# Performance work log

Hardware: AMD Instinct MI355X
Metric: run time of the kernel (lower is better)

The kernel has to match this reference:

```python
import jax, jax.numpy as jnp
import numpy as np

B = 64      # batch
T = 32      # frames per clip
H = 256     # hidden_dim
NMAX = 64   # max boxes per batch element


def _n_per_frame():
    rng = np.random.default_rng(0)
    return rng.integers(32, NMAX + 1, size=B)  # each n <= NMAX


def setup_inputs() -> dict:
    n = _n_per_frame()
    N = int(n.sum())  # total boxes across batch (~3072)
    key = jax.random.key(0)
    k1, k2, k3 = jax.random.split(key, 3)
    bbox = jax.random.uniform(k1, (N * T, 4), dtype=jnp.float32)
    W1 = jax.random.normal(k2, (4, 128), dtype=jnp.float32) * 0.5
    b1 = jnp.zeros((128,), jnp.float32)
    W2 = jax.random.normal(k3, (128, H), dtype=jnp.float32) * 0.0884  # ~1/sqrt(128)
    b2 = jnp.zeros((H,), jnp.float32)
    return {
        "bbox": bbox,
        "W1": W1, "b1": b1, "W2": W2, "b2": b2,
        "n_per_frame": jnp.asarray(n, jnp.int32),
        "n_max": NMAX,
    }


def reference(bbox, W1, b1, W2, b2, n_per_frame, n_max):
    N = bbox.shape[0] // T  # static total box count
    # tiny MLP: 4 -> 128 -> H
    pos = (jax.nn.relu(bbox @ W1 + b1) @ W2 + b2).reshape(N, T, H)
    # ragged scatter into padded (B*n_max, T, H) tensor
    frame_id = jnp.repeat(jnp.arange(B), n_per_frame, total_repeat_length=N)  # [N]
    starts = jnp.cumsum(n_per_frame) - n_per_frame                            # exclusive cumsum [B]
    local = jnp.arange(N) - starts[frame_id]                                  # slot within frame
    tgt = frame_id * n_max + local                                            # [N] unique targets
    pos_pad = jnp.zeros((B * n_max, T, H), pos.dtype).at[tgt].set(pos)
    # (B, n_max, T, H) -> (B, T, n_max, H) -> (B*T, n_max, H) -> (n_max, B*T, H)
    out = (pos_pad.reshape(B, n_max, T, H)
           .transpose(0, 2, 1, 3)
           .reshape(B * T, n_max, H)
           .transpose(1, 0, 2))
    return out
```

## Files before the change

kernel.cpp:

```cpp
#include <hip/hip_runtime.h>

#define B_ 64
#define T_ 32
#define H_ 256
#define NMAX_ 64
#define TILES 2048
#define GRID 512
#define BLOCK 256
#define SROW 260

typedef __attribute__((ext_vector_type(8))) short short8;
typedef __attribute__((ext_vector_type(4))) float f32x4;

__device__ __forceinline__ short f2bf(float f) {
    unsigned u = __builtin_bit_cast(unsigned, f);
    u = (u + 0x7fffu + ((u >> 16) & 1u)) >> 16;
    return (short)u;
}

__device__ __forceinline__ void barrier_nodrain() {
    asm volatile("s_waitcnt lgkmcnt(0)\n\ts_barrier" ::: "memory");
}

__global__ __launch_bounds__(BLOCK, 2)
void pe_fused(const float* __restrict__ bbox,
              const float* __restrict__ W1,
              const float* __restrict__ b1,
              const float* __restrict__ W2,
              const float* __restrict__ b2,
              const int*   __restrict__ npf,
              float* __restrict__ out,
              int NT)
{
    __shared__ float W1s[512];
    __shared__ float b1s[128];
    __shared__ int   s_n[64];
    __shared__ int   s_start[64];
    __shared__ short Hs[64 * 136];
    __shared__ float stage[32 * SROW];

    const int tid  = threadIdx.x;
    const int wave = tid >> 6;
    const int lane = tid & 63;
    const int q    = lane >> 4;
    const int m16  = lane & 15;

    if (tid < 256) { W1s[tid] = W1[tid]; W1s[tid + 256] = W1[tid + 256]; }
    if (tid < 128) b1s[tid] = b1[tid];

    if (wave == 0) {
        int v = npf[lane];
        s_n[lane] = v;
        int s = v;
#pragma unroll
        for (int d = 1; d < 64; d <<= 1) {
            int u = __shfl_up(s, d, 64);
            if (lane >= d) s += u;
        }
        s_start[lane] = s - v;
    }

    short8 Wf[4][4];
    float4 b2q[4];
#pragma unroll
    for (int ct = 0; ct < 4; ++ct) {
        b2q[ct] = *(const float4*)(b2 + wave * 64 + ct * 16 + q * 4);
#pragma unroll
        for (int kc = 0; kc < 4; ++kc) {
            const int k0 = kc * 32 + q * 8;
            short8 f;
#pragma unroll
            for (int jj = 0; jj < 8; ++jj)
                f[jj] = f2bf(W2[(k0 + jj) * H_ + wave * 64 + ct * 16 + m16]);
            Wf[ct][kc] = f;
        }
    }
    __syncthreads();

    const int r4 = tid >> 2;
    const int c4 = tid & 3;

    float4 bb[4];
#pragma unroll
    for (int i = 0; i < 4; ++i) {
        const int tt = blockIdx.x + i * GRID;
        const int b  = tt >> 5;
        const int l0 = (tt & 31) * 2;
        const int g  = (s_start[b] + l0) * T_ + r4;
        bb[i] = make_float4(0.f, 0.f, 0.f, 0.f);
        if (g < NT) bb[i] = *(const float4*)(bbox + g * 4);
    }

#pragma unroll
    for (int i = 0; i < 4; ++i) {
        const int tt = blockIdx.x + i * GRID;
        const int b  = tt >> 5;
        const int l0 = (tt & 31) * 2;
        const int nb = s_n[b];

        const int ob0 = (l0 * (B_ * T_) + b * T_) * H_;
        const int ob1 = ob0 + (B_ * T_) * H_;

        if (l0 >= nb) {
            const float4 z = make_float4(0.f, 0.f, 0.f, 0.f);
#pragma unroll
            for (int rr = 0; rr < 16; ++rr) {
                const int r = rr * 4 + wave;
                float* dst = out + (r < 32 ? ob0 + r * H_ : ob1 + (r - 32) * H_);
                *(float4*)(dst + lane * 4) = z;
            }
            continue;
        }

        {
            const float4 bv = bb[i];
            short* hrow = &Hs[r4 * 136 + c4 * 32];
#pragma unroll
            for (int w = 0; w < 4; ++w) {
                short8 hv;
#pragma unroll
                for (int jj = 0; jj < 8; ++jj) {
                    const int h = c4 * 32 + w * 8 + jj;
                    float v = b1s[h];
                    v = fmaf(bv.x, W1s[h],       v);
                    v = fmaf(bv.y, W1s[128 + h], v);
                    v = fmaf(bv.z, W1s[256 + h], v);
                    v = fmaf(bv.w, W1s[384 + h], v);
                    v = fmaxf(v, 0.f);
                    hv[jj] = f2bf(v);
                }
                *(short8*)(hrow + w * 8) = hv;
            }
        }
        barrier_nodrain();

        f32x4 acc[4][4];
#pragma unroll
        for (int ct = 0; ct < 4; ++ct)
#pragma unroll
            for (int rt = 0; rt < 4; ++rt)
                acc[ct][rt] = (f32x4){0.f, 0.f, 0.f, 0.f};

#pragma unroll
        for (int kc = 0; kc < 4; ++kc) {
            short8 hf[4];
#pragma unroll
            for (int rt = 0; rt < 4; ++rt)
                hf[rt] = *(const short8*)&Hs[(rt * 16 + m16) * 136 + kc * 32 + q * 8];
#pragma unroll
            for (int ct = 0; ct < 4; ++ct)
#pragma unroll
                for (int rt = 0; rt < 4; ++rt)
                    acc[ct][rt] = __builtin_amdgcn_mfma_f32_16x16x32_bf16(
                        Wf[ct][kc], hf[rt], acc[ct][rt], 0, 0, 0);
        }

        const bool v1 = (l0 + 1) < nb;
#pragma unroll
        for (int half = 0; half < 2; ++half) {
            const int obh = half ? ob1 : ob0;
            if (half == 1 && !v1) {
                const float4 z = make_float4(0.f, 0.f, 0.f, 0.f);
#pragma unroll
                for (int j = 0; j < 8; ++j)
                    *(float4*)(out + obh + (wave * 8 + j) * H_ + lane * 4) = z;
                continue;
            }
#pragma unroll
            for (int rt2 = 0; rt2 < 2; ++rt2) {
                const int rt = 2 * half + rt2;
                const int u  = rt2 * 16 + m16;
#pragma unroll
                for (int ct = 0; ct < 4; ++ct) {
                    const f32x4 d = acc[ct][rt];
                    float4 v = make_float4(d[0] + b2q[ct].x, d[1] + b2q[ct].y,
                                           d[2] + b2q[ct].z, d[3] + b2q[ct].w);
                    *(float4*)&stage[u * SROW + wave * 64 + ct * 16 + q * 4] = v;
                }
            }
            barrier_nodrain();
#pragma unroll
            for (int j = 0; j < 8; ++j) {
                const int u = wave * 8 + j;
                const float4 v = *(const float4*)&stage[u * SROW + lane * 4];
                *(float4*)(out + obh + u * H_ + lane * 4) = v;
            }
            barrier_nodrain();
        }
    }
}

extern "C" void kernel_launch(void* const* d_in, const int* in_sizes, int n_in,
                              void* d_out, int out_size, void* d_ws, size_t ws_size,
                              hipStream_t stream)
{
    const float* bbox = (const float*)d_in[0];
    const float* W1   = (const float*)d_in[1];
    const float* b1   = (const float*)d_in[2];
    const float* W2   = (const float*)d_in[3];
    const float* b2   = (const float*)d_in[4];
    const int*   npf  = (const int*)d_in[5];
    const int NT = in_sizes[0] / 4;

    pe_fused<<<GRID, BLOCK, 0, stream>>>(bbox, W1, b1, W2, b2, npf,
                                         (float*)d_out, NT);
}
```

Before: 152.6 us.

## Split output columns across block pairs and store MFMA results directly

Raises the grid from 512 to 2048 blocks. Each pair of blocks now splits the 256 output columns into two halves, so each block runs two tile iterations instead of four, with half as many W2 fragments and accumulators held in registers. The LDS staging buffer and its barriers before the global stores are removed, and accumulators are written straight to global memory as 16-byte stores. Accumulators start from b2, and W1 is packed as float4 in LDS. The trade-offs are less coalesced stores (16 rows of 64-byte segments per wave instruction), the layer-1 MLP computed twice per tile (once per column half), and no bbox prefetch across iterations.

```diff
diff --git a/kernel.cpp b/kernel.cpp
--- a/kernel.cpp
+++ b/kernel.cpp
@@ -4,10 +4,9 @@
 #define T_ 32
 #define H_ 256
 #define NMAX_ 64
-#define TILES 2048
-#define GRID 512
+#define GRID 2048
 #define BLOCK 256
-#define SROW 260
+#define HSROW 136
 
 typedef __attribute__((ext_vector_type(8))) short short8;
 typedef __attribute__((ext_vector_type(4))) float f32x4;
@@ -22,7 +21,7 @@
     asm volatile("s_waitcnt lgkmcnt(0)\n\ts_barrier" ::: "memory");
 }
 
-__global__ __launch_bounds__(BLOCK, 2)
+__global__ __launch_bounds__(BLOCK, 4)
 void pe_fused(const float* __restrict__ bbox,
               const float* __restrict__ W1,
               const float* __restrict__ b1,
@@ -32,12 +31,11 @@
               float* __restrict__ out,
               int NT)
 {
-    __shared__ float W1s[512];
-    __shared__ float b1s[128];
-    __shared__ int   s_n[64];
-    __shared__ int   s_start[64];
-    __shared__ short Hs[64 * 136];
-    __shared__ float stage[32 * SROW];
+    __shared__ float4 W1t[128];
+    __shared__ float  b1s[128];
+    __shared__ int    s_n[64];
+    __shared__ int    s_start[64];
+    __shared__ short  Hs[64 * HSROW];
 
     const int tid  = threadIdx.x;
     const int wave = tid >> 6;
@@ -45,9 +43,13 @@
     const int q    = lane >> 4;
     const int m16  = lane & 15;
 
-    if (tid < 256) { W1s[tid] = W1[tid]; W1s[tid + 256] = W1[tid + 256]; }
-    if (tid < 128) b1s[tid] = b1[tid];
+    const int ch = blockIdx.x & 1;
+    const int p0 = blockIdx.x >> 1;
 
+    if (tid < 128) {
+        W1t[tid] = make_float4(W1[tid], W1[128 + tid], W1[256 + tid], W1[384 + tid]);
+        b1s[tid] = b1[tid];
+    }
     if (wave == 0) {
         int v = npf[lane];
         s_n[lane] = v;
@@ -60,72 +62,68 @@
         s_start[lane] = s - v;
     }
 
-    short8 Wf[4][4];
-    float4 b2q[4];
+    const int colw = ch * 128 + wave * 32;
+    short8 Wf[2][4];
 #pragma unroll
-    for (int ct = 0; ct < 4; ++ct) {
-        b2q[ct] = *(const float4*)(b2 + wave * 64 + ct * 16 + q * 4);
+    for (int ct = 0; ct < 2; ++ct)
 #pragma unroll
         for (int kc = 0; kc < 4; ++kc) {
-            const int k0 = kc * 32 + q * 8;
             short8 f;
 #pragma unroll
             for (int jj = 0; jj < 8; ++jj)
-                f[jj] = f2bf(W2[(k0 + jj) * H_ + wave * 64 + ct * 16 + m16]);
+                f[jj] = f2bf(W2[(kc * 32 + q * 8 + jj) * H_ + colw + ct * 16 + m16]);
             Wf[ct][kc] = f;
         }
-    }
-    __syncthreads();
+    float4 b2v[2];
+#pragma unroll
+    for (int ct = 0; ct < 2; ++ct)
+        b2v[ct] = *(const float4*)(b2 + colw + ct * 16 + q * 4);
 
-    const int r4 = tid >> 2;
-    const int c4 = tid & 3;
-
-    float4 bb[4];
-#pragma unroll
-    for (int i = 0; i < 4; ++i) {
-        const int tt = blockIdx.x + i * GRID;
-        const int b  = tt >> 5;
-        const int l0 = (tt & 31) * 2;
-        const int g  = (s_start[b] + l0) * T_ + r4;
-        bb[i] = make_float4(0.f, 0.f, 0.f, 0.f);
-        if (g < NT) bb[i] = *(const float4*)(bbox + g * 4);
-    }
+    barrier_nodrain();
 
 #pragma unroll
-    for (int i = 0; i < 4; ++i) {
-        const int tt = blockIdx.x + i * GRID;
-        const int b  = tt >> 5;
-        const int l0 = (tt & 31) * 2;
-        const int nb = s_n[b];
+    for (int it = 0; it < 2; ++it) {
+        const int pair = it ? (p0 + 1024) : p0;
+        const int b    = pair >> 5;
+        const int l0   = (pair & 31) * 2;
+        const int nb   = s_n[b];
 
         const int ob0 = (l0 * (B_ * T_) + b * T_) * H_;
         const int ob1 = ob0 + (B_ * T_) * H_;
 
         if (l0 >= nb) {
             const float4 z = make_float4(0.f, 0.f, 0.f, 0.f);
+            const int col = ch * 128 + (lane & 31) * 4;
 #pragma unroll
-            for (int rr = 0; rr < 16; ++rr) {
-                const int r = rr * 4 + wave;
-                float* dst = out + (r < 32 ? ob0 + r * H_ : ob1 + (r - 32) * H_);
-                *(float4*)(dst + lane * 4) = z;
+            for (int j = 0; j < 8; ++j) {
+                const int r = wave * 16 + j * 2 + (lane >> 5);
+                float* dst = out + (r < 32 ? ob0 + r * H_ : ob1 + (r - 32) * H_) + col;
+                *(float4*)dst = z;
             }
             continue;
         }
 
+        barrier_nodrain();
+
         {
-            const float4 bv = bb[i];
-            short* hrow = &Hs[r4 * 136 + c4 * 32];
+            const int r4 = tid >> 2;
+            const int c4 = tid & 3;
+            const int g  = (s_start[b] + l0) * T_ + r4;
+            float4 bv = make_float4(0.f, 0.f, 0.f, 0.f);
+            if (g < NT) bv = *(const float4*)(bbox + g * 4);
+            short* hrow = &Hs[r4 * HSROW + c4 * 32];
 #pragma unroll
             for (int w = 0; w < 4; ++w) {
                 short8 hv;
 #pragma unroll
                 for (int jj = 0; jj < 8; ++jj) {
                     const int h = c4 * 32 + w * 8 + jj;
+                    const float4 wv = W1t[h];
                     float v = b1s[h];
-                    v = fmaf(bv.x, W1s[h],       v);
-                    v = fmaf(bv.y, W1s[128 + h], v);
-                    v = fmaf(bv.z, W1s[256 + h], v);
-                    v = fmaf(bv.w, W1s[384 + h], v);
+                    v = fmaf(bv.x, wv.x, v);
+                    v = fmaf(bv.y, wv.y, v);
+                    v = fmaf(bv.z, wv.z, v);
+                    v = fmaf(bv.w, wv.w, v);
                     v = fmaxf(v, 0.f);
                     hv[jj] = f2bf(v);
                 }
@@ -134,21 +132,21 @@
         }
         barrier_nodrain();
 
-        f32x4 acc[4][4];
+        f32x4 acc[2][4];
 #pragma unroll
-        for (int ct = 0; ct < 4; ++ct)
+        for (int ct = 0; ct < 2; ++ct)
 #pragma unroll
             for (int rt = 0; rt < 4; ++rt)
-                acc[ct][rt] = (f32x4){0.f, 0.f, 0.f, 0.f};
+                acc[ct][rt] = (f32x4){b2v[ct].x, b2v[ct].y, b2v[ct].z, b2v[ct].w};
 
 #pragma unroll
         for (int kc = 0; kc < 4; ++kc) {
             short8 hf[4];
 #pragma unroll
             for (int rt = 0; rt < 4; ++rt)
-                hf[rt] = *(const short8*)&Hs[(rt * 16 + m16) * 136 + kc * 32 + q * 8];
+                hf[rt] = *(const short8*)&Hs[(rt * 16 + m16) * HSROW + kc * 32 + q * 8];
 #pragma unroll
-            for (int ct = 0; ct < 4; ++ct)
+            for (int ct = 0; ct < 2; ++ct)
 #pragma unroll
                 for (int rt = 0; rt < 4; ++rt)
                     acc[ct][rt] = __builtin_amdgcn_mfma_f32_16x16x32_bf16(
@@ -157,35 +155,21 @@
 
         const bool v1 = (l0 + 1) < nb;
 #pragma unroll
-        for (int half = 0; half < 2; ++half) {
-            const int obh = half ? ob1 : ob0;
-            if (half == 1 && !v1) {
-                const float4 z = make_float4(0.f, 0.f, 0.f, 0.f);
+        for (int ct = 0; ct < 2; ++ct) {
+            const int cb = colw + ct * 16 + q * 4;
 #pragma unroll
-                for (int j = 0; j < 8; ++j)
-                    *(float4*)(out + obh + (wave * 8 + j) * H_ + lane * 4) = z;
-                continue;
+            for (int rt = 0; rt < 4; ++rt) {
+                const int t = (rt & 1) * 16 + m16;
+                float* dst = out + (rt < 2 ? ob0 : ob1) + t * H_ + cb;
+                float4 val;
+                if (rt >= 2 && !v1) {
+                    val = make_float4(0.f, 0.f, 0.f, 0.f);
+                } else {
+                    const f32x4 a = acc[ct][rt];
+                    val = make_float4(a[0], a[1], a[2], a[3]);
+                }
+                *(float4*)dst = val;
             }
-#pragma unroll
-            for (int rt2 = 0; rt2 < 2; ++rt2) {
-                const int rt = 2 * half + rt2;
-                const int u  = rt2 * 16 + m16;
-#pragma unroll
-                for (int ct = 0; ct < 4; ++ct) {
-                    const f32x4 d = acc[ct][rt];
-                    float4 v = make_float4(d[0] + b2q[ct].x, d[1] + b2q[ct].y,
-                                           d[2] + b2q[ct].z, d[3] + b2q[ct].w);
-                    *(float4*)&stage[u * SROW + wave * 64 + ct * 16 + q * 4] = v;
-                }
-            }
-            barrier_nodrain();
-#pragma unroll
-            for (int j = 0; j < 8; ++j) {
-                const int u = wave * 8 + j;
-                const float4 v = *(const float4*)&stage[u * SROW + lane * 4];
-                *(float4*)(out + obh + u * H_ + lane * 4) = v;
-            }
-            barrier_nodrain();
         }
     }
 }
```

New measurement: 165.4 us. 1.08x slower.

## Alias H and staging LDS buffers, raise occupancy, and double grid size

Applied to the files above, without the earlier changes.

Shares one LDS buffer between the bf16 hidden activations and the output staging area, with an extra barrier after the MFMA loop so the buffer can be reused safely. This cuts LDS per block so three blocks per CU fit, and the grid doubles to 1024 blocks with two tiles each. Other changes: the bias b2 moves into LDS and seeds the accumulators, and W1 is stored transposed as float4 so each hidden value needs one LDS load. The trade-off is an extra barrier per tile, the W2 fragment load and bf16 conversion done by twice as many blocks, and register pressure under the tighter launch bound.

```diff
diff --git a/kernel.cpp b/kernel.cpp
--- a/kernel.cpp
+++ b/kernel.cpp
@@ -4,9 +4,9 @@
 #define T_ 32
 #define H_ 256
 #define NMAX_ 64
-#define TILES 2048
-#define GRID 512
+#define GRID 1024
 #define BLOCK 256
+#define HSROW 136
 #define SROW 260
 
 typedef __attribute__((ext_vector_type(8))) short short8;
@@ -22,7 +22,7 @@
     asm volatile("s_waitcnt lgkmcnt(0)\n\ts_barrier" ::: "memory");
 }
 
-__global__ __launch_bounds__(BLOCK, 2)
+__global__ __launch_bounds__(BLOCK, 3)
 void pe_fused(const float* __restrict__ bbox,
               const float* __restrict__ W1,
               const float* __restrict__ b1,
@@ -32,12 +32,15 @@
               float* __restrict__ out,
               int NT)
 {
-    __shared__ float W1s[512];
-    __shared__ float b1s[128];
-    __shared__ int   s_n[64];
-    __shared__ int   s_start[64];
-    __shared__ short Hs[64 * 136];
-    __shared__ float stage[32 * SROW];
+    __shared__ float4 W1t[128];
+    __shared__ float  b1s[128];
+    __shared__ float  b2s[256];
+    __shared__ int    s_n[64];
+    __shared__ int    s_start[64];
+    __shared__ float  smem[32 * SROW];
+
+    short* const Hs    = (short*)smem;
+    float* const stage = smem;
 
     const int tid  = threadIdx.x;
     const int wave = tid >> 6;
@@ -45,9 +48,11 @@
     const int q    = lane >> 4;
     const int m16  = lane & 15;
 
-    if (tid < 256) { W1s[tid] = W1[tid]; W1s[tid + 256] = W1[tid + 256]; }
-    if (tid < 128) b1s[tid] = b1[tid];
-
+    if (tid < 128) {
+        W1t[tid] = make_float4(W1[tid], W1[128 + tid], W1[256 + tid], W1[384 + tid]);
+        b1s[tid] = b1[tid];
+    }
+    b2s[tid] = b2[tid];
     if (wave == 0) {
         int v = npf[lane];
         s_n[lane] = v;
@@ -61,10 +66,8 @@
     }
 
     short8 Wf[4][4];
-    float4 b2q[4];
-#pragma unroll
-    for (int ct = 0; ct < 4; ++ct) {
-        b2q[ct] = *(const float4*)(b2 + wave * 64 + ct * 16 + q * 4);
+#pragma unroll
+    for (int ct = 0; ct < 4; ++ct)
 #pragma unroll
         for (int kc = 0; kc < 4; ++kc) {
             const int k0 = kc * 32 + q * 8;
@@ -74,15 +77,14 @@
                 f[jj] = f2bf(W2[(k0 + jj) * H_ + wave * 64 + ct * 16 + m16]);
             Wf[ct][kc] = f;
         }
-    }
     __syncthreads();
 
     const int r4 = tid >> 2;
     const int c4 = tid & 3;
 
-    float4 bb[4];
-#pragma unroll
-    for (int i = 0; i < 4; ++i) {
+    float4 bb[2];
+#pragma unroll
+    for (int i = 0; i < 2; ++i) {
         const int tt = blockIdx.x + i * GRID;
         const int b  = tt >> 5;
         const int l0 = (tt & 31) * 2;
@@ -92,7 +94,7 @@
     }
 
 #pragma unroll
-    for (int i = 0; i < 4; ++i) {
+    for (int i = 0; i < 2; ++i) {
         const int tt = blockIdx.x + i * GRID;
         const int b  = tt >> 5;
         const int l0 = (tt & 31) * 2;
@@ -114,18 +116,19 @@
 
         {
             const float4 bv = bb[i];
-            short* hrow = &Hs[r4 * 136 + c4 * 32];
+            short* hrow = &Hs[r4 * HSROW + c4 * 32];
 #pragma unroll
             for (int w = 0; w < 4; ++w) {
                 short8 hv;
 #pragma unroll
                 for (int jj = 0; jj < 8; ++jj) {
                     const int h = c4 * 32 + w * 8 + jj;
+                    const float4 wv = W1t[h];
                     float v = b1s[h];
-                    v = fmaf(bv.x, W1s[h],       v);
-                    v = fmaf(bv.y, W1s[128 + h], v);
-                    v = fmaf(bv.z, W1s[256 + h], v);
-                    v = fmaf(bv.w, W1s[384 + h], v);
+                    v = fmaf(bv.x, wv.x, v);
+                    v = fmaf(bv.y, wv.y, v);
+                    v = fmaf(bv.z, wv.z, v);
+                    v = fmaf(bv.w, wv.w, v);
                     v = fmaxf(v, 0.f);
                     hv[jj] = f2bf(v);
                 }
@@ -136,17 +139,19 @@
 
         f32x4 acc[4][4];
 #pragma unroll
-        for (int ct = 0; ct < 4; ++ct)
+        for (int ct = 0; ct < 4; ++ct) {
+            const float4 bq = *(const float4*)&b2s[wave * 64 + ct * 16 + q * 4];
 #pragma unroll
             for (int rt = 0; rt < 4; ++rt)
-                acc[ct][rt] = (f32x4){0.f, 0.f, 0.f, 0.f};
+                acc[ct][rt] = (f32x4){bq.x, bq.y, bq.z, bq.w};
+        }
 
 #pragma unroll
         for (int kc = 0; kc < 4; ++kc) {
             short8 hf[4];
 #pragma unroll
             for (int rt = 0; rt < 4; ++rt)
-                hf[rt] = *(const short8*)&Hs[(rt * 16 + m16) * 136 + kc * 32 + q * 8];
+                hf[rt] = *(const short8*)&Hs[(rt * 16 + m16) * HSROW + kc * 32 + q * 8];
 #pragma unroll
             for (int ct = 0; ct < 4; ++ct)
 #pragma unroll
@@ -154,6 +159,7 @@
                     acc[ct][rt] = __builtin_amdgcn_mfma_f32_16x16x32_bf16(
                         Wf[ct][kc], hf[rt], acc[ct][rt], 0, 0, 0);
         }
+        barrier_nodrain();
 
         const bool v1 = (l0 + 1) < nb;
 #pragma unroll
@@ -173,9 +179,8 @@
 #pragma unroll
                 for (int ct = 0; ct < 4; ++ct) {
                     const f32x4 d = acc[ct][rt];
-                    float4 v = make_float4(d[0] + b2q[ct].x, d[1] + b2q[ct].y,
-                                           d[2] + b2q[ct].z, d[3] + b2q[ct].w);
-                    *(float4*)&stage[u * SROW + wave * 64 + ct * 16 + q * 4] = v;
+                    *(float4*)&stage[u * SROW + wave * 64 + ct * 16 + q * 4] =
+                        make_float4(d[0], d[1], d[2], d[3]);
                 }
             }
             barrier_nodrain();
```

New measurement: 161.8 us. +6.0%, slower.
